# Optimization experiments

Measured on AMD Instinct MI355X. Metric: run time of the kernel, lower is better.

## Reference

```python
import jax, jax.numpy as jnp
import numpy as np

BLOCK = 128  # fp8 block-quant block size (block_size = [128, 128])


def _dequant(w, s):
    # w: [E, O, I] fp8-simulated values; s: [E, O, I//BLOCK] per-block scales
    # (scale_inv already repeat_interleaved along the out dim by the module).
    E, O, I = w.shape
    nb = s.shape[-1]
    bs = I // nb
    return (w.reshape(E, O, nb, bs) * s[..., None]).reshape(E, O, I)


def setup_inputs() -> dict:
    key = jax.random.key(0)
    ks = jax.random.split(key, 8)
    B, S, H, I, E = 1, 512, 2048, 768, 16
    return {
        "hidden_states": jax.random.normal(ks[0], (B, S, H), jnp.float32),
        "gate_w": jax.random.normal(ks[1], (E, H), jnp.float32) * 0.02,
        "w1": jax.random.normal(ks[2], (E, I, H), jnp.float32),
        "w1_scale": jax.random.uniform(ks[3], (E, I, H // BLOCK), jnp.float32, 0.005, 0.02),
        "w3": jax.random.normal(ks[4], (E, I, H), jnp.float32),
        "w3_scale": jax.random.uniform(ks[5], (E, I, H // BLOCK), jnp.float32, 0.005, 0.02),
        "w2": jax.random.normal(ks[6], (E, H, I), jnp.float32),
        "w2_scale": jax.random.uniform(ks[7], (E, H, I // BLOCK), jnp.float32, 0.005, 0.02),
        "top_k": 2,
    }


def reference(hidden_states, gate_w, w1, w1_scale, w3, w3_scale, w2, w2_scale, top_k):
    B, S, H = hidden_states.shape
    x = hidden_states.reshape(-1, H)           # [T, H]
    T = x.shape[0]
    E = gate_w.shape[0]

    # Router: sigmoid scores, top-k, sum-normalization (norm_topk_prob=False)
    router_logits = x @ gate_w.T               # [T, E]
    scores = jax.nn.sigmoid(router_logits.astype(jnp.float32))
    top_w, top_i = jax.lax.top_k(scores, top_k)
    top_w = top_w / jnp.sum(top_w, axis=-1, keepdims=True)

    # Dense combine matrix [T, E] (top-k sparse in the real kernel)
    combine = jnp.zeros((T, E), x.dtype).at[jnp.arange(T)[:, None], top_i].add(
        top_w.astype(x.dtype))

    # Inline block dequantization of fp8 weights
    w1d = _dequant(w1, w1_scale)               # [E, I, H]
    w3d = _dequant(w3, w3_scale)               # [E, I, H]
    w2d = _dequant(w2, w2_scale)               # [E, H, I]

    # SwiGLU expert MLPs (grouped GEMM expressed densely over experts)
    g = jnp.einsum('th,eih->eti', x, w1d)      # gate proj
    u = jnp.einsum('th,eih->eti', x, w3d)      # up proj
    a = jax.nn.silu(g) * u                     # [E, T, I]
    expert_out = jnp.einsum('eti,ehi->eth', a, w2d)  # down proj [E, T, H]

    y = jnp.einsum('te,eth->th', combine, expert_out)
    return y.reshape(B, S, H)
```

## Files before the change

kernel.cpp:

```cpp
#include <hip/hip_runtime.h>
#include <math.h>

#define H 2048
#define II 768
#define TT 512
#define EE 16
#define BK 64

typedef float f32x4 __attribute__((ext_vector_type(4)));
typedef short s16x8 __attribute__((ext_vector_type(8)));
typedef unsigned short u16;
typedef u16 u16x8 __attribute__((ext_vector_type(8)));

__device__ __forceinline__ u16 f2bf(float f) {
  unsigned int u = __float_as_uint(f);
  u += 0x7fffu + ((u >> 16) & 1u);
  return (u16)(u >> 16);
}

__global__ void router_kernel(const float* __restrict__ x, const float* __restrict__ gw,
                              int* __restrict__ counts, int* __restrict__ topi,
                              float* __restrict__ topw, int* __restrict__ pos) {
  int t = blockIdx.x;
  int tid = threadIdx.x;
  int wave = tid >> 6, lane = tid & 63;
  __shared__ float logits[EE];
  const float* xt = x + (size_t)t * H;
  for (int e = wave * 4; e < wave * 4 + 4; ++e) {
    const float* ge = gw + (size_t)e * H;
    float p = 0.f;
    for (int h = lane * 4; h < H; h += 64 * 4) {
      f32x4 xv = *(const f32x4*)(xt + h);
      f32x4 gv = *(const f32x4*)(ge + h);
      p += xv[0]*gv[0] + xv[1]*gv[1] + xv[2]*gv[2] + xv[3]*gv[3];
    }
    #pragma unroll
    for (int off = 32; off > 0; off >>= 1) p += __shfl_down(p, off);
    if (lane == 0) logits[e] = p;
  }
  __syncthreads();
  if (tid == 0) {
    float s[EE];
    #pragma unroll
    for (int e = 0; e < EE; ++e) s[e] = 1.f / (1.f + expf(-logits[e]));
    int i0 = 0;
    for (int e = 1; e < EE; ++e) if (s[e] > s[i0]) i0 = e;
    int i1 = -1;
    for (int e = 0; e < EE; ++e) {
      if (e == i0) continue;
      if (i1 < 0 || s[e] > s[i1]) i1 = e;
    }
    float w0 = s[i0], w1v = s[i1];
    float inv = 1.f / (w0 + w1v);
    w0 *= inv; w1v *= inv;
    topi[t*2+0] = i0; topi[t*2+1] = i1;
    topw[t*2+0] = w0; topw[t*2+1] = w1v;
    pos[t*2+0] = atomicAdd(&counts[i0], 1);
    pos[t*2+1] = atomicAdd(&counts[i1], 1);
  }
}

__global__ void prefix_kernel(const int* __restrict__ counts, int* __restrict__ base) {
  int s = 0;
  for (int e = 0; e < EE; ++e) { base[e] = s; s += counts[e]; }
  base[EE] = s;
}

__global__ void gather_kernel(const float* __restrict__ x, const int* __restrict__ topi,
                              const float* __restrict__ topw, const int* __restrict__ pos,
                              const int* __restrict__ base, u16* __restrict__ Xg,
                              int* __restrict__ tok_of, float* __restrict__ wt_of) {
  int t = blockIdx.x, slot = blockIdx.y;
  int e = topi[t*2 + slot];
  int row = base[e] + pos[t*2 + slot];
  if (threadIdx.x == 0) { tok_of[row] = t; wt_of[row] = topw[t*2 + slot]; }
  const float* xt = x + (size_t)t * H;
  u16* dst = Xg + (size_t)row * H;
  int h = threadIdx.x * 8;
  f32x4 v0 = *(const f32x4*)(xt + h);
  f32x4 v1 = *(const f32x4*)(xt + h + 4);
  u16x8 o;
  o[0]=f2bf(v0[0]); o[1]=f2bf(v0[1]); o[2]=f2bf(v0[2]); o[3]=f2bf(v0[3]);
  o[4]=f2bf(v1[0]); o[5]=f2bf(v1[1]); o[6]=f2bf(v1[2]); o[7]=f2bf(v1[3]);
  *(u16x8*)(dst + h) = o;
}

__global__ __launch_bounds__(256, 4) void gemm1_kernel(
    const u16* __restrict__ Xg,
    const float* __restrict__ w1, const float* __restrict__ w1s,
    const float* __restrict__ w3, const float* __restrict__ w3s,
    const int* __restrict__ counts, const int* __restrict__ base,
    u16* __restrict__ Ag) {
  const int e = blockIdx.y;
  const int cnt = counts[e];
  if (cnt == 0) return;
  const int n0 = blockIdx.x * 16;
  const int b0 = base[e];
  const int tid = threadIdx.x;
  const int lane = tid & 63;
  const int w = tid >> 6;

  __shared__ __align__(16) u16 As[64 * 64];
  __shared__ __align__(16) u16 Bs[2][16 * 64];

  const int rA = tid >> 3;
  const int cA = (tid & 7) << 3;
  const int cAs = cA ^ ((rA & 7) << 3);
  const int isB3 = tid >> 7;
  const int rB = (tid & 127) >> 3;
  const int cBs = cA ^ ((rB & 7) << 3);
  const float* wsrc = (isB3 ? w3 : w1) + (size_t)(e * II + n0 + rB) * H + cA;
  const float* ssrc = (isB3 ? w3s : w1s) + (size_t)(e * II + n0 + rB) * (H / 128);
  u16* bdst = &Bs[isB3][rB * 64 + cBs];

  const int arow = w * 16 + (lane & 15);
  const int acol0 = (lane >> 4) << 3;
  const int brow = lane & 15;
  const int aswz = (arow & 7) << 3;
  const int bswz = (brow & 7) << 3;

  const int nmt = (cnt + 63) >> 6;
  for (int mt = 0; mt < nmt; ++mt) {
    const u16* asrc = Xg + (size_t)(b0 + mt * 64 + rA) * H + cA;
    f32x4 accg = {}, accu = {};
    s16x8 a0, a1; f32x4 bv0, bv1; float sc;
    a0 = *(const s16x8*)(asrc);
    a1 = *(const s16x8*)(asrc + (size_t)32 * H);
    bv0 = *(const f32x4*)(wsrc);
    bv1 = *(const f32x4*)(wsrc + 4);
    sc = ssrc[0];
    {
      *(s16x8*)(As + rA * 64 + cAs) = a0;
      *(s16x8*)(As + (rA + 32) * 64 + cAs) = a1;
      u16x8 ob;
      ob[0]=f2bf(bv0[0]*sc); ob[1]=f2bf(bv0[1]*sc); ob[2]=f2bf(bv0[2]*sc); ob[3]=f2bf(bv0[3]*sc);
      ob[4]=f2bf(bv1[0]*sc); ob[5]=f2bf(bv1[1]*sc); ob[6]=f2bf(bv1[2]*sc); ob[7]=f2bf(bv1[3]*sc);
      *(u16x8*)bdst = ob;
    }
    __syncthreads();
    for (int t = 0; t < H / BK; ++t) {
      const bool notlast = (t + 1 < H / BK);
      if (notlast) {
        const int k1 = (t + 1) * BK;
        a0 = *(const s16x8*)(asrc + k1);
        a1 = *(const s16x8*)(asrc + (size_t)32 * H + k1);
        bv0 = *(const f32x4*)(wsrc + k1);
        bv1 = *(const f32x4*)(wsrc + k1 + 4);
        sc = ssrc[k1 >> 7];
      }
      #pragma unroll
      for (int ks = 0; ks < 2; ++ks) {
        const int ac = ks * 32 + acol0;
        s16x8 af  = *(const s16x8*)(As + arow * 64 + (ac ^ aswz));
        const int bix = brow * 64 + (ac ^ bswz);
        s16x8 b1f = *(const s16x8*)(Bs[0] + bix);
        s16x8 b3f = *(const s16x8*)(Bs[1] + bix);
        accg = __builtin_amdgcn_mfma_f32_16x16x32_bf16(af, b1f, accg, 0, 0, 0);
        accu = __builtin_amdgcn_mfma_f32_16x16x32_bf16(af, b3f, accu, 0, 0, 0);
      }
      __syncthreads();
      if (notlast) {
        *(s16x8*)(As + rA * 64 + cAs) = a0;
        *(s16x8*)(As + (rA + 32) * 64 + cAs) = a1;
        u16x8 ob;
        ob[0]=f2bf(bv0[0]*sc); ob[1]=f2bf(bv0[1]*sc); ob[2]=f2bf(bv0[2]*sc); ob[3]=f2bf(bv0[3]*sc);
        ob[4]=f2bf(bv1[0]*sc); ob[5]=f2bf(bv1[1]*sc); ob[6]=f2bf(bv1[2]*sc); ob[7]=f2bf(bv1[3]*sc);
        *(u16x8*)bdst = ob;
      }
      __syncthreads();
    }
    const int col = n0 + (lane & 15);
    #pragma unroll
    for (int r4 = 0; r4 < 4; ++r4) {
      int mrow = mt * 64 + w * 16 + ((lane >> 4) << 2) + r4;
      if (mrow < cnt) {
        float g = accg[r4], u = accu[r4];
        float a = g / (1.f + expf(-g)) * u;
        Ag[(size_t)(b0 + mrow) * II + col] = f2bf(a);
      }
    }
  }
}

__global__ __launch_bounds__(256, 4) void gemm2_kernel(
    const u16* __restrict__ Ag,
    const float* __restrict__ w2, const float* __restrict__ w2s,
    const int* __restrict__ counts, const int* __restrict__ base,
    const int* __restrict__ tok_of, const float* __restrict__ wt_of,
    float* __restrict__ y) {
  const int e = blockIdx.y;
  const int cnt = counts[e];
  if (cnt == 0) return;
  const int n0 = blockIdx.x * 32;
  const int b0 = base[e];
  const int tid = threadIdx.x;
  const int lane = tid & 63;
  const int w = tid >> 6;

  __shared__ __align__(16) u16 As[64 * 64];
  __shared__ __align__(16) u16 Bs[32 * 64];

  const int rA = tid >> 3;
  const int cA = (tid & 7) << 3;
  const int cAs = cA ^ ((rA & 7) << 3);
  const int rB = tid >> 3;
  const int cBs = cA ^ ((rB & 7) << 3);
  const float* wsrc = w2 + (size_t)(e * H + n0 + rB) * II + cA;
  const float* ssrc = w2s + (size_t)(e * H + n0 + rB) * (II / 128);
  u16* bdst = &Bs[rB * 64 + cBs];

  const int arow = w * 16 + (lane & 15);
  const int acol0 = (lane >> 4) << 3;
  const int brow = lane & 15;
  const int aswz = (arow & 7) << 3;

  const int nmt = (cnt + 63) >> 6;
  for (int mt = 0; mt < nmt; ++mt) {
    const u16* asrc = Ag + (size_t)(b0 + mt * 64 + rA) * II + cA;
    f32x4 acc0 = {}, acc1 = {};
    s16x8 a0, a1; f32x4 bv0, bv1; float sc;
    a0 = *(const s16x8*)(asrc);
    a1 = *(const s16x8*)(asrc + (size_t)32 * II);
    bv0 = *(const f32x4*)(wsrc);
    bv1 = *(const f32x4*)(wsrc + 4);
    sc = ssrc[0];
    {
      *(s16x8*)(As + rA * 64 + cAs) = a0;
      *(s16x8*)(As + (rA + 32) * 64 + cAs) = a1;
      u16x8 ob;
      ob[0]=f2bf(bv0[0]*sc); ob[1]=f2bf(bv0[1]*sc); ob[2]=f2bf(bv0[2]*sc); ob[3]=f2bf(bv0[3]*sc);
      ob[4]=f2bf(bv1[0]*sc); ob[5]=f2bf(bv1[1]*sc); ob[6]=f2bf(bv1[2]*sc); ob[7]=f2bf(bv1[3]*sc);
      *(u16x8*)bdst = ob;
    }
    __syncthreads();
    for (int t = 0; t < II / BK; ++t) {
      const bool notlast = (t + 1 < II / BK);
      if (notlast) {
        const int k1 = (t + 1) * BK;
        a0 = *(const s16x8*)(asrc + k1);
        a1 = *(const s16x8*)(asrc + (size_t)32 * II + k1);
        bv0 = *(const f32x4*)(wsrc + k1);
        bv1 = *(const f32x4*)(wsrc + k1 + 4);
        sc = ssrc[k1 >> 7];
      }
      #pragma unroll
      for (int ks = 0; ks < 2; ++ks) {
        const int ac = ks * 32 + acol0;
        s16x8 af  = *(const s16x8*)(As + arow * 64 + (ac ^ aswz));
        s16x8 b0f = *(const s16x8*)(Bs + brow * 64 + (ac ^ ((brow & 7) << 3)));
        const int br1 = brow + 16;
        s16x8 b1f = *(const s16x8*)(Bs + br1 * 64 + (ac ^ ((br1 & 7) << 3)));
        acc0 = __builtin_amdgcn_mfma_f32_16x16x32_bf16(af, b0f, acc0, 0, 0, 0);
        acc1 = __builtin_amdgcn_mfma_f32_16x16x32_bf16(af, b1f, acc1, 0, 0, 0);
      }
      __syncthreads();
      if (notlast) {
        *(s16x8*)(As + rA * 64 + cAs) = a0;
        *(s16x8*)(As + (rA + 32) * 64 + cAs) = a1;
        u16x8 ob;
        ob[0]=f2bf(bv0[0]*sc); ob[1]=f2bf(bv0[1]*sc); ob[2]=f2bf(bv0[2]*sc); ob[3]=f2bf(bv0[3]*sc);
        ob[4]=f2bf(bv1[0]*sc); ob[5]=f2bf(bv1[1]*sc); ob[6]=f2bf(bv1[2]*sc); ob[7]=f2bf(bv1[3]*sc);
        *(u16x8*)bdst = ob;
      }
      __syncthreads();
    }
    #pragma unroll
    for (int r4 = 0; r4 < 4; ++r4) {
      int mrow = mt * 64 + w * 16 + ((lane >> 4) << 2) + r4;
      if (mrow < cnt) {
        int grow = b0 + mrow;
        int t = tok_of[grow];
        float wt = wt_of[grow];
        atomicAdd(y + (size_t)t * H + n0 + (lane & 15), acc0[r4] * wt);
        atomicAdd(y + (size_t)t * H + n0 + 16 + (lane & 15), acc1[r4] * wt);
      }
    }
  }
}

extern "C" void kernel_launch(void* const* d_in, const int* in_sizes, int n_in,
                              void* d_out, int out_size, void* d_ws, size_t ws_size,
                              hipStream_t stream) {
  const float* x   = (const float*)d_in[0];
  const float* gw  = (const float*)d_in[1];
  const float* w1  = (const float*)d_in[2];
  const float* w1s = (const float*)d_in[3];
  const float* w3  = (const float*)d_in[4];
  const float* w3s = (const float*)d_in[5];
  const float* w2  = (const float*)d_in[6];
  const float* w2s = (const float*)d_in[7];
  float* y = (float*)d_out;

  char* ws = (char*)d_ws;
  int*   counts = (int*)(ws + 0);
  int*   basep  = (int*)(ws + 64);
  int*   topi   = (int*)(ws + 256);
  float* topw   = (float*)(ws + 256 + 4096);
  int*   pos    = (int*)(ws + 256 + 8192);
  int*   tok_of = (int*)(ws + 256 + 12288);
  float* wt_of  = (float*)(ws + 256 + 16384);
  u16*   Xg     = (u16*)(ws + 256 + 20480);
  u16*   Ag     = (u16*)(ws + 256 + 20480 + (size_t)1152*H*2);

  hipMemsetAsync(counts, 0, 64, stream);
  hipMemsetAsync(y, 0, (size_t)out_size * sizeof(float), stream);

  router_kernel<<<TT, 256, 0, stream>>>(x, gw, counts, topi, topw, pos);
  prefix_kernel<<<1, 1, 0, stream>>>(counts, basep);
  gather_kernel<<<dim3(TT, 2), 256, 0, stream>>>(x, topi, topw, pos, basep, Xg, tok_of, wt_of);
  gemm1_kernel<<<dim3(II / 16, EE), 256, 0, stream>>>(Xg, w1, w1s, w3, w3s, counts, basep, Ag);
  gemm2_kernel<<<dim3(H / 32, EE), 256, 0, stream>>>(Ag, w2, w2s, counts, basep, tok_of, wt_of, y);
}
```

Baseline: 132.3 us.

## Split-K both expert GEMMs and move SiLU into a separate reduction kernel

Result: slower. 139.6 us (+5.6%).

```diff
diff --git a/kernel.cpp b/kernel.cpp
--- a/kernel.cpp
+++ b/kernel.cpp
@@ -10,6 +10,7 @@
 typedef float f32x4 __attribute__((ext_vector_type(4)));
 typedef short s16x8 __attribute__((ext_vector_type(8)));
 typedef unsigned short u16;
+typedef u16 u16x4 __attribute__((ext_vector_type(4)));
 typedef u16 u16x8 __attribute__((ext_vector_type(8)));
 
 __device__ __forceinline__ u16 f2bf(float f) {
@@ -85,16 +86,19 @@
   *(u16x8*)(dst + h) = o;
 }
 
-__global__ __launch_bounds__(256, 4) void gemm1_kernel(
+__global__ __launch_bounds__(256, 8) void gemm1_kernel(
     const u16* __restrict__ Xg,
     const float* __restrict__ w1, const float* __restrict__ w1s,
     const float* __restrict__ w3, const float* __restrict__ w3s,
     const int* __restrict__ counts, const int* __restrict__ base,
-    u16* __restrict__ Ag) {
+    float* __restrict__ slab) {
+  const int bx = blockIdx.x;
+  const int nc = bx >> 2, kc = bx & 3;
   const int e = blockIdx.y;
   const int cnt = counts[e];
   if (cnt == 0) return;
-  const int n0 = blockIdx.x * 16;
+  const int n0 = nc * 16;
+  const int k0 = kc * 512;
   const int b0 = base[e];
   const int tid = threadIdx.x;
   const int lane = tid & 63;
@@ -109,8 +113,8 @@
   const int isB3 = tid >> 7;
   const int rB = (tid & 127) >> 3;
   const int cBs = cA ^ ((rB & 7) << 3);
-  const float* wsrc = (isB3 ? w3 : w1) + (size_t)(e * II + n0 + rB) * H + cA;
-  const float* ssrc = (isB3 ? w3s : w1s) + (size_t)(e * II + n0 + rB) * (H / 128);
+  const float* wsrc = (isB3 ? w3 : w1) + (size_t)(e * II + n0 + rB) * H + k0 + cA;
+  const float* ssrc = (isB3 ? w3s : w1s) + (size_t)(e * II + n0 + rB) * (H / 128) + kc * 4;
   u16* bdst = &Bs[isB3][rB * 64 + cBs];
 
   const int arow = w * 16 + (lane & 15);
@@ -119,9 +123,12 @@
   const int aswz = (arow & 7) << 3;
   const int bswz = (brow & 7) << 3;
 
+  float* outG = slab + ((size_t)kc) * ((size_t)1024 * II);
+  float* outU = slab + ((size_t)(4 + kc)) * ((size_t)1024 * II);
+
   const int nmt = (cnt + 63) >> 6;
   for (int mt = 0; mt < nmt; ++mt) {
-    const u16* asrc = Xg + (size_t)(b0 + mt * 64 + rA) * H + cA;
+    const u16* asrc = Xg + (size_t)(b0 + mt * 64 + rA) * H + k0 + cA;
     f32x4 accg = {}, accu = {};
     s16x8 a0, a1; f32x4 bv0, bv1; float sc;
     a0 = *(const s16x8*)(asrc);
@@ -138,8 +145,8 @@
       *(u16x8*)bdst = ob;
     }
     __syncthreads();
-    for (int t = 0; t < H / BK; ++t) {
-      const bool notlast = (t + 1 < H / BK);
+    for (int t = 0; t < 512 / BK; ++t) {
+      const bool notlast = (t + 1 < 512 / BK);
       if (notlast) {
         const int k1 = (t + 1) * BK;
         a0 = *(const s16x8*)(asrc + k1);
@@ -174,24 +181,45 @@
     for (int r4 = 0; r4 < 4; ++r4) {
       int mrow = mt * 64 + w * 16 + ((lane >> 4) << 2) + r4;
       if (mrow < cnt) {
-        float g = accg[r4], u = accu[r4];
-        float a = g / (1.f + expf(-g)) * u;
-        Ag[(size_t)(b0 + mrow) * II + col] = f2bf(a);
-      }
-    }
-  }
-}
-
-__global__ __launch_bounds__(256, 4) void gemm2_kernel(
+        outG[(size_t)(b0 + mrow) * II + col] = accg[r4];
+        outU[(size_t)(b0 + mrow) * II + col] = accu[r4];
+      }
+    }
+  }
+}
+
+__global__ void silu_kernel(const float* __restrict__ slab, u16* __restrict__ Ag) {
+  const size_t i = ((size_t)blockIdx.x * 256 + threadIdx.x) * 4;
+  const float* G = slab;
+  const float* U = slab + (size_t)4 * 1024 * II;
+  f32x4 g = {}, u = {};
+  #pragma unroll
+  for (int kc = 0; kc < 4; ++kc) {
+    g += *(const f32x4*)(G + (size_t)kc * 1024 * II + i);
+    u += *(const f32x4*)(U + (size_t)kc * 1024 * II + i);
+  }
+  u16x4 o;
+  #pragma unroll
+  for (int j = 0; j < 4; ++j) {
+    float a = g[j] / (1.f + expf(-g[j])) * u[j];
+    o[j] = f2bf(a);
+  }
+  *(u16x4*)(Ag + i) = o;
+}
+
+__global__ __launch_bounds__(256, 8) void gemm2_kernel(
     const u16* __restrict__ Ag,
     const float* __restrict__ w2, const float* __restrict__ w2s,
     const int* __restrict__ counts, const int* __restrict__ base,
     const int* __restrict__ tok_of, const float* __restrict__ wt_of,
     float* __restrict__ y) {
+  const int bx = blockIdx.x;
+  const int nc = bx >> 1, kc = bx & 1;
   const int e = blockIdx.y;
   const int cnt = counts[e];
   if (cnt == 0) return;
-  const int n0 = blockIdx.x * 32;
+  const int n0 = nc * 32;
+  const int k0 = kc * 384;
   const int b0 = base[e];
   const int tid = threadIdx.x;
   const int lane = tid & 63;
@@ -205,8 +233,8 @@
   const int cAs = cA ^ ((rA & 7) << 3);
   const int rB = tid >> 3;
   const int cBs = cA ^ ((rB & 7) << 3);
-  const float* wsrc = w2 + (size_t)(e * H + n0 + rB) * II + cA;
-  const float* ssrc = w2s + (size_t)(e * H + n0 + rB) * (II / 128);
+  const float* wsrc = w2 + (size_t)(e * H + n0 + rB) * II + k0 + cA;
+  const float* ssrc = w2s + (size_t)(e * H + n0 + rB) * (II / 128) + kc * 3;
   u16* bdst = &Bs[rB * 64 + cBs];
 
   const int arow = w * 16 + (lane & 15);
@@ -216,7 +244,7 @@
 
   const int nmt = (cnt + 63) >> 6;
   for (int mt = 0; mt < nmt; ++mt) {
-    const u16* asrc = Ag + (size_t)(b0 + mt * 64 + rA) * II + cA;
+    const u16* asrc = Ag + (size_t)(b0 + mt * 64 + rA) * II + k0 + cA;
     f32x4 acc0 = {}, acc1 = {};
     s16x8 a0, a1; f32x4 bv0, bv1; float sc;
     a0 = *(const s16x8*)(asrc);
@@ -233,8 +261,8 @@
       *(u16x8*)bdst = ob;
     }
     __syncthreads();
-    for (int t = 0; t < II / BK; ++t) {
-      const bool notlast = (t + 1 < II / BK);
+    for (int t = 0; t < 384 / BK; ++t) {
+      const bool notlast = (t + 1 < 384 / BK);
       if (notlast) {
         const int k1 = (t + 1) * BK;
         a0 = *(const s16x8*)(asrc + k1);
@@ -299,8 +327,9 @@
   int*   pos    = (int*)(ws + 256 + 8192);
   int*   tok_of = (int*)(ws + 256 + 12288);
   float* wt_of  = (float*)(ws + 256 + 16384);
-  u16*   Xg     = (u16*)(ws + 256 + 20480);
-  u16*   Ag     = (u16*)(ws + 256 + 20480 + (size_t)1152*H*2);
+  u16*   Xg     = (u16*)(ws + 20736);
+  u16*   Ag     = (u16*)(ws + 20736 + 4718592);
+  float* slab   = (float*)(ws + 20736 + 4718592 + 1769472);
 
   hipMemsetAsync(counts, 0, 64, stream);
   hipMemsetAsync(y, 0, (size_t)out_size * sizeof(float), stream);
@@ -308,6 +337,7 @@
   router_kernel<<<TT, 256, 0, stream>>>(x, gw, counts, topi, topw, pos);
   prefix_kernel<<<1, 1, 0, stream>>>(counts, basep);
   gather_kernel<<<dim3(TT, 2), 256, 0, stream>>>(x, topi, topw, pos, basep, Xg, tok_of, wt_of);
-  gemm1_kernel<<<dim3(II / 16, EE), 256, 0, stream>>>(Xg, w1, w1s, w3, w3s, counts, basep, Ag);
-  gemm2_kernel<<<dim3(H / 32, EE), 256, 0, stream>>>(Ag, w2, w2s, counts, basep, tok_of, wt_of, y);
-}
+  gemm1_kernel<<<dim3(48 * 4, EE), 256, 0, stream>>>(Xg, w1, w1s, w3, w3s, counts, basep, slab);
+  silu_kernel<<<(1024 * II) / (256 * 4), 256, 0, stream>>>(slab, Ag);
+  gemm2_kernel<<<dim3(64 * 2, EE), 256, 0, stream>>>(Ag, w2, w2s, counts, basep, tok_of, wt_of, y);
+}
```
